# Kernel optimization log

Measured on AMD Instinct MI355X. Metric: run time of the kernel, lower is better.

## Reference

```python
import jax, jax.numpy as jnp
import numpy as np

B, E, H, SEQ = 4096, 512, 512, 128


def setup_inputs() -> dict:
    key = jax.random.key(0)
    ks = jax.random.split(key, 7)
    s = 1.0 / np.sqrt(H)  # PyTorch LSTM init scale
    return {
        "start_emb": jax.random.normal(ks[0], (B, 1, E), dtype=jnp.float32),
        "h0": jax.random.normal(ks[1], (1, B, H), dtype=jnp.float32),
        "c0": jax.random.normal(ks[2], (1, B, H), dtype=jnp.float32),
        "w_ih": jax.random.normal(ks[3], (4 * H, E), dtype=jnp.float32) * s,
        "w_hh": jax.random.normal(ks[4], (4 * H, H), dtype=jnp.float32) * s,
        "b_ih": jax.random.normal(ks[5], (4 * H,), dtype=jnp.float32) * s,
        "b_hh": jax.random.normal(ks[6], (4 * H,), dtype=jnp.float32) * s,
        "seq_length": SEQ,
    }


def reference(start_emb, h0, c0, w_ih, w_hh, b_ih, b_hh, seq_length):
    # start_emb: [B, 1, E] -- identical input every step, so precompute its projection once.
    x = start_emb[:, 0, :]                       # [B, E]
    x_proj = x @ w_ih.T + b_ih + b_hh            # [B, 4H], constant across steps
    hdim = w_hh.shape[1]

    def step(carry, _):
        h, c = carry                              # each [B, H]
        gates = x_proj + h @ w_hh.T               # [B, 4H]
        i, f, g, o = jnp.split(gates, 4, axis=-1) # PyTorch gate order i,f,g,o
        i = jax.nn.sigmoid(i)
        f = jax.nn.sigmoid(f)
        g = jnp.tanh(g)
        o = jax.nn.sigmoid(o)
        c = f * c + i * g
        h = o * jnp.tanh(c)
        return (h, c), None

    (h, c), _ = jax.lax.scan(step, (h0[0], c0[0]), None, length=seq_length)
    # Return final (h_n, c_n) with the [num_layers=1, B, H] leading dim, as PyTorch does.
    return h[None], c[None]
```

## Files before the change

### kernel.cpp

```cpp
#include <hip/hip_runtime.h>
#include <hip/hip_bf16.h>

#define BATCH 4096
#define KD    512
#define NG    2048
#define SEQLEN 128

typedef __attribute__((ext_vector_type(8))) short short8;
typedef __attribute__((ext_vector_type(4))) float floatx4;

#define HWREG_XCC_ID (20 | (0 << 6) | ((4 - 1) << 11))

__device__ __forceinline__ void gld16(const void* g, void* l) {
  __builtin_amdgcn_global_load_lds(
      (const __attribute__((address_space(1))) void*)g,
      (__attribute__((address_space(3))) void*)l, 16, 0, 0);
}

__device__ __forceinline__ float fast_sig(float x) {
  return __builtin_amdgcn_rcpf(1.0f + __expf(-x));
}
__device__ __forceinline__ float fast_tanh(float x) {
  return 1.0f - 2.0f * __builtin_amdgcn_rcpf(1.0f + __expf(2.0f * x));
}

__device__ __forceinline__ unsigned pack_bf16(float lo, float hi) {
  unsigned ul = (unsigned)__builtin_bit_cast(unsigned short, __float2bfloat16(lo));
  unsigned uh = (unsigned)__builtin_bit_cast(unsigned short, __float2bfloat16(hi));
  return (uh << 16) | ul;
}
__device__ __forceinline__ float unpack_lo(unsigned u) {
  u <<= 16; return __builtin_bit_cast(float, u);
}
__device__ __forceinline__ float unpack_hi(unsigned u) {
  u &= 0xffff0000u; return __builtin_bit_cast(float, u);
}

__device__ __forceinline__ void load_panel(const short* __restrict__ W, int bn,
                                           short* __restrict__ lWB, int tid) {
#pragma unroll
  for (int i = 0; i < 16; ++i) {
    int q = i * 512 + tid;
    int row = q >> 6, c = q & 63;
    int c0 = (c & 56) | ((c & 7) ^ (row & 7));
    gld16(W + (size_t)(bn + row) * KD + c0 * 8, lWB + q * 8);
  }
}

__device__ __forceinline__ void gemm_panel(const short* __restrict__ A,
                                           const short* __restrict__ lWB,
                                           short* __restrict__ lA,
                                           floatx4 acc[4][4],
                                           int bm, int lane, int wm, int wn,
                                           int tid) {
#pragma unroll 1
  for (int kt = 0; kt < 8; ++kt) {
    const int k0 = kt * 64;
#pragma unroll
    for (int i = 0; i < 4; ++i) {
      int q = i * 512 + tid;
      int row = q >> 3, cs = q & 7;
      int cc = cs ^ (row & 7);
      gld16(A + (size_t)(bm + row) * KD + k0 + cc * 8, lA + q * 8);
    }
    __syncthreads();
#pragma unroll
    for (int ks = 0; ks < 2; ++ks) {
      short8 a[4], b[4];
#pragma unroll
      for (int mi = 0; mi < 4; ++mi) {
        int arow = wm * 64 + mi * 16 + (lane & 15);
        int ch = (ks * 4 + (lane >> 4)) ^ (arow & 7);
        a[mi] = *(const short8*)&lA[arow * 64 + ch * 8];
      }
#pragma unroll
      for (int j = 0; j < 4; ++j) {
        int brow = wn * 64 + j * 16 + (lane & 15);
        int c = kt * 8 + ks * 4 + (lane >> 4);
        int cc = (c & 56) | ((c & 7) ^ (brow & 7));
        b[j] = *(const short8*)&lWB[brow * 512 + cc * 8];
      }
#pragma unroll
      for (int mi = 0; mi < 4; ++mi)
#pragma unroll
        for (int j = 0; j < 4; ++j)
          acc[mi][j] =
              __builtin_amdgcn_mfma_f32_16x16x32_bf16(a[mi], b[j], acc[mi][j], 0, 0, 0);
    }
    __syncthreads();
  }
}

template <int TBM, int TBN, int NT>
__device__ __forceinline__ void gemm_tile(const short* __restrict__ A,
                                          const short* __restrict__ Bw,
                                          floatx4 acc[4][4],
                                          short* lA, short* lB,
                                          int bm, int bn,
                                          int lane, int wm, int wn, int tid) {
#pragma unroll 1
  for (int kt = 0; kt < KD / 64; ++kt) {
    const int k0 = kt * 64;
#pragma unroll
    for (int i = 0; i < TBM * 8 / NT; ++i) {
      int q = i * NT + tid;
      int row = q >> 3, cs = q & 7;
      int cc = cs ^ (row & 7);
      gld16(A + (size_t)(bm + row) * KD + k0 + cc * 8, lA + q * 8);
    }
#pragma unroll
    for (int i = 0; i < TBN * 8 / NT; ++i) {
      int q = i * NT + tid;
      int row = q >> 3, cs = q & 7;
      int cc = cs ^ (row & 7);
      gld16(Bw + (size_t)(bn + row) * KD + k0 + cc * 8, lB + q * 8);
    }
    __syncthreads();
#pragma unroll
    for (int ks = 0; ks < 2; ++ks) {
      short8 a[4], b[4];
#pragma unroll
      for (int mi = 0; mi < 4; ++mi) {
        int arow = wm * 64 + mi * 16 + (lane & 15);
        int ch = (ks * 4 + (lane >> 4)) ^ (arow & 7);
        a[mi] = *(const short8*)&lA[arow * 64 + ch * 8];
      }
#pragma unroll
      for (int j = 0; j < 4; ++j) {
        int brow = wn * 64 + j * 16 + (lane & 15);
        int ch = (ks * 4 + (lane >> 4)) ^ (brow & 7);
        b[j] = *(const short8*)&lB[brow * 64 + ch * 8];
      }
#pragma unroll
      for (int mi = 0; mi < 4; ++mi)
#pragma unroll
        for (int j = 0; j < 4; ++j)
          acc[mi][j] =
              __builtin_amdgcn_mfma_f32_16x16x32_bf16(a[mi], b[j], acc[mi][j], 0, 0, 0);
    }
    __syncthreads();
  }
}

__device__ __forceinline__ void group_barrier_xcd(unsigned* cnt, unsigned target) {
  __syncthreads();
  if (threadIdx.x == 0) {
    __hip_atomic_fetch_add(cnt, 1u, __ATOMIC_RELAXED, __HIP_MEMORY_SCOPE_AGENT);
    unsigned guard = 0;
    while (__hip_atomic_load(cnt, __ATOMIC_RELAXED, __HIP_MEMORY_SCOPE_AGENT) <
               target &&
           ++guard < (1u << 20)) {
      __builtin_amdgcn_s_sleep(1);
    }
    asm volatile("buffer_inv sc0" ::: "memory");
    asm volatile("s_waitcnt vmcnt(0)" ::: "memory");
  }
  __syncthreads();
}

__global__ __launch_bounds__(512, 1) void lstm_persist(
    const short* __restrict__ xbf,
    const short* __restrict__ wih,
    const short* __restrict__ whh,
    const float* __restrict__ biasp,
    const float* __restrict__ c0,
    short* __restrict__ hA, short* __restrict__ hB,
    float* __restrict__ outH, float* __restrict__ outC,
    unsigned* __restrict__ sync_area) {
  extern __shared__ __align__(16) char dsm[];
  short* lWB = (short*)dsm;
  short* lA  = (short*)(dsm + 131072);

  const int tid = threadIdx.x;
  const int lane = tid & 63;
  const int wid = tid >> 6;
  const int wm = wid >> 1;
  const int wn = wid & 1;

  if (tid == 0) {
    int px = __builtin_amdgcn_s_getreg(HWREG_XCC_ID) & 7;
    unsigned r = __hip_atomic_fetch_add(&sync_area[px], 1u, __ATOMIC_RELAXED,
                                        __HIP_MEMORY_SCOPE_AGENT);
    ((int*)lA)[0] = px * 2 + (int)((r >> 4) & 1);
    ((int*)lA)[1] = (int)(r & 15);
  }
  __syncthreads();
  const int gid = ((int*)lA)[0];
  const int by  = ((int*)lA)[1];
  __syncthreads();
  const int bm = gid * 256;
  const int bn = by * 128;
  unsigned* gcnt = sync_area + 256 + gid * 32;

  const int houter = by * 2 + wn;
  const int hcol = houter * 16 + (lane & 15);
  const int rb = houter * 64 + (lane & 15);

  load_panel(wih, bn, lWB, tid);
  __syncthreads();
  floatx4 acc[4][4] = {};
  gemm_panel(xbf, lWB, lA, acc, bm, lane, wm, wn, tid);

  const float b0 = biasp[rb], b1 = biasp[rb + 16], b2 = biasp[rb + 32],
              b3 = biasp[rb + 48];
  unsigned xprP[4][4][2];
  float creg[4][4];
#pragma unroll
  for (int mi = 0; mi < 4; ++mi) {
    const int mrow0 = bm + wm * 64 + mi * 16 + (lane >> 4) * 4;
#pragma unroll
    for (int reg = 0; reg < 4; ++reg) {
      xprP[mi][reg][0] = pack_bf16(acc[mi][0][reg] + b0, acc[mi][1][reg] + b1);
      xprP[mi][reg][1] = pack_bf16(acc[mi][2][reg] + b2, acc[mi][3][reg] + b3);
      creg[mi][reg] = c0[(size_t)(mrow0 + reg) * KD + hcol];
    }
  }

  load_panel(whh, bn, lWB, tid);
  __syncthreads();

#pragma unroll 1
  for (int t = 0; t < SEQLEN; ++t) {
    const short* hin = (t & 1) ? hB : hA;
    short* hout = (t & 1) ? hA : hB;

#pragma unroll
    for (int mi = 0; mi < 4; ++mi)
#pragma unroll
      for (int j = 0; j < 4; ++j)
        acc[mi][j] = floatx4{0.f, 0.f, 0.f, 0.f};

    gemm_panel(hin, lWB, lA, acc, bm, lane, wm, wn, tid);

#pragma unroll
    for (int mi = 0; mi < 4; ++mi) {
      const int mrow0 = bm + wm * 64 + mi * 16 + (lane >> 4) * 4;
#pragma unroll
      for (int reg = 0; reg < 4; ++reg) {
        const int m = mrow0 + reg;
        float gi = acc[mi][0][reg] + unpack_lo(xprP[mi][reg][0]);
        float gf = acc[mi][1][reg] + unpack_hi(xprP[mi][reg][0]);
        float gg = acc[mi][2][reg] + unpack_lo(xprP[mi][reg][1]);
        float go = acc[mi][3][reg] + unpack_hi(xprP[mi][reg][1]);
        float si = fast_sig(gi);
        float sf = fast_sig(gf);
        float tg = fast_tanh(gg);
        float so = fast_sig(go);
        float cn = sf * creg[mi][reg] + si * tg;
        creg[mi][reg] = cn;
        float hn = so * fast_tanh(cn);
        const size_t ci = (size_t)m * KD + hcol;
        ((__hip_bfloat16*)hout)[ci] = __float2bfloat16(hn);
        if (t == SEQLEN - 1) {
          outH[ci] = hn;
          outC[ci] = cn;
        }
      }
    }
    if (t != SEQLEN - 1) group_barrier_xcd(gcnt, 16u * (unsigned)(t + 1));
  }
}

__global__ __launch_bounds__(256, 2) void lstm_step(
    const short* __restrict__ hin, __hip_bfloat16* __restrict__ hout_bf,
    const short* __restrict__ W, const float* __restrict__ xp,
    float* __restrict__ c, float* __restrict__ hout_f32) {
  __shared__ __align__(16) short lA[128 * 64];
  __shared__ __align__(16) short lB[128 * 64];
  const int tid = threadIdx.x;
  const int lane = tid & 63;
  const int wid = tid >> 6;
  const int wm = wid >> 1, wn = wid & 1;
  const int bm = blockIdx.x * 128, bn = blockIdx.y * 128;

  floatx4 acc[4][4] = {};
  gemm_tile<128, 128, 256>(hin, W, acc, lA, lB, bm, bn, lane, wm, wn, tid);

  const int houter = blockIdx.y * 2 + wn;
  const int hcol = houter * 16 + (lane & 15);
  const int rb = houter * 64 + (lane & 15);
#pragma unroll
  for (int mi = 0; mi < 4; ++mi) {
    const int mrow0 = bm + wm * 64 + mi * 16 + (lane >> 4) * 4;
#pragma unroll
    for (int reg = 0; reg < 4; ++reg) {
      const int m = mrow0 + reg;
      const float* xpr = xp + (size_t)m * NG + rb;
      float si = fast_sig(acc[mi][0][reg] + xpr[0]);
      float sf = fast_sig(acc[mi][1][reg] + xpr[16]);
      float tg = fast_tanh(acc[mi][2][reg] + xpr[32]);
      float so = fast_sig(acc[mi][3][reg] + xpr[48]);
      const int ci = m * KD + hcol;
      float cn = sf * c[ci] + si * tg;
      c[ci] = cn;
      float hn = so * fast_tanh(cn);
      hout_bf[ci] = __float2bfloat16(hn);
      if (hout_f32) hout_f32[ci] = hn;
    }
  }
}

__global__ __launch_bounds__(256, 2) void xproj_gemm(
    const short* __restrict__ xbf, const short* __restrict__ Wih,
    const float* __restrict__ biasp, float* __restrict__ xp) {
  __shared__ __align__(16) short lA[128 * 64];
  __shared__ __align__(16) short lB[128 * 64];
  const int tid = threadIdx.x;
  const int lane = tid & 63;
  const int wid = tid >> 6;
  const int wm = wid >> 1, wn = wid & 1;
  const int bm = blockIdx.x * 128, bn = blockIdx.y * 128;

  floatx4 acc[4][4] = {};
  gemm_tile<128, 128, 256>(xbf, Wih, acc, lA, lB, bm, bn, lane, wm, wn, tid);

  const int houter = blockIdx.y * 2 + wn;
  const int rb = houter * 64 + (lane & 15);
  const float b0 = biasp[rb], b1 = biasp[rb + 16], b2 = biasp[rb + 32],
              b3 = biasp[rb + 48];
#pragma unroll
  for (int mi = 0; mi < 4; ++mi) {
    const int mrow0 = bm + wm * 64 + mi * 16 + (lane >> 4) * 4;
#pragma unroll
    for (int reg = 0; reg < 4; ++reg) {
      float* xpr = xp + (size_t)(mrow0 + reg) * NG + rb;
      xpr[0]  = acc[mi][0][reg] + b0;
      xpr[16] = acc[mi][1][reg] + b1;
      xpr[32] = acc[mi][2][reg] + b2;
      xpr[48] = acc[mi][3][reg] + b3;
    }
  }
}

__global__ void permw_k(const float* __restrict__ w,
                        __hip_bfloat16* __restrict__ o) {
  int idx = blockIdx.x * 256 + threadIdx.x;
  int r = idx >> 9, k = idx & 511;
  int hout = r >> 6, g = (r >> 4) & 3, hin = r & 15;
  o[idx] = __float2bfloat16(w[(size_t)((g << 9) + hout * 16 + hin) * 512 + k]);
}

__global__ void bias_k(const float* __restrict__ bi, const float* __restrict__ bh,
                       float* __restrict__ o) {
  int r = blockIdx.x * 256 + threadIdx.x;
  int hout = r >> 6, g = (r >> 4) & 3, hin = r & 15;
  int n = (g << 9) + hout * 16 + hin;
  o[r] = bi[n] + bh[n];
}

__global__ void f2bf_k(const float* __restrict__ in,
                       __hip_bfloat16* __restrict__ out, int n) {
  int i = blockIdx.x * 256 + threadIdx.x;
  if (i < n) out[i] = __float2bfloat16(in[i]);
}

extern "C" void kernel_launch(void* const* d_in, const int* in_sizes, int n_in,
                              void* d_out, int out_size, void* d_ws, size_t ws_size,
                              hipStream_t stream) {
  const float* start_emb = (const float*)d_in[0];
  const float* h0 = (const float*)d_in[1];
  const float* c0 = (const float*)d_in[2];
  const float* w_ih = (const float*)d_in[3];
  const float* w_hh = (const float*)d_in[4];
  const float* b_ih = (const float*)d_in[5];
  const float* b_hh = (const float*)d_in[6];

  char* ws = (char*)d_ws;
  __hip_bfloat16* whh_p = (__hip_bfloat16*)(ws);
  __hip_bfloat16* wih_p = (__hip_bfloat16*)(ws + (2ll << 20));
  __hip_bfloat16* xbf   = (__hip_bfloat16*)(ws + (4ll << 20));
  __hip_bfloat16* hbufA = (__hip_bfloat16*)(ws + (8ll << 20));
  __hip_bfloat16* hbufB = (__hip_bfloat16*)(ws + (12ll << 20));
  float* biasp          = (float*)(ws + (16ll << 20));
  unsigned* sync_area   = (unsigned*)(ws + (16ll << 20) + 65536);
  float* xp             = (float*)(ws + (17ll << 20));

  float* outH = (float*)d_out;
  float* outC = (float*)d_out + (size_t)BATCH * KD;

  permw_k<<<4096, 256, 0, stream>>>(w_hh, whh_p);
  permw_k<<<4096, 256, 0, stream>>>(w_ih, wih_p);
  bias_k<<<8, 256, 0, stream>>>(b_ih, b_hh, biasp);
  f2bf_k<<<8192, 256, 0, stream>>>(start_emb, xbf, BATCH * KD);
  f2bf_k<<<8192, 256, 0, stream>>>(h0, hbufA, BATCH * KD);
  (void)hipMemsetAsync(sync_area, 0, 8192, stream);

  const short* a_xbf = (const short*)xbf;
  const short* a_wih = (const short*)wih_p;
  const short* a_whh = (const short*)whh_p;
  const float* a_bias = biasp;
  const float* a_c0 = c0;
  short* a_hA = (short*)hbufA;
  short* a_hB = (short*)hbufB;
  float* a_outH = outH;
  float* a_outC = outC;
  unsigned* a_sync = sync_area;
  void* args[] = {&a_xbf, &a_wih, &a_whh, &a_bias, &a_c0,
                  &a_hA, &a_hB, &a_outH, &a_outC, &a_sync};
  hipError_t e = hipLaunchCooperativeKernel((const void*)lstm_persist,
                                            dim3(256), dim3(512), args,
                                            163840, stream);
  if (e != hipSuccess) {
    (void)hipMemcpyAsync(outC, c0, (size_t)BATCH * KD * sizeof(float),
                         hipMemcpyDeviceToDevice, stream);
    dim3 grid(BATCH / 128, NG / 128);
    xproj_gemm<<<grid, 256, 0, stream>>>((const short*)xbf, (const short*)wih_p,
                                         biasp, xp);
    for (int t = 0; t < SEQLEN; ++t) {
      const short* hin = (const short*)((t & 1) ? hbufB : hbufA);
      __hip_bfloat16* hout = (t & 1) ? hbufA : hbufB;
      lstm_step<<<grid, 256, 0, stream>>>(hin, hout, (const short*)whh_p, xp,
                                          outC, (t == SEQLEN - 1) ? outH : nullptr);
    }
  }
}
```

Before: 1.605 ms.

## Keep a quarter of the weight panel in registers and double-buffer A tiles

Each wave now holds one 16-row slice of its recurrent weight panel in VGPRs (16 short8 per lane), and only the remaining 96 rows go to LDS. This shrinks the LDS panel so the A tile can be double-buffered: the next k-tile load is issued before computing on the current one, and the per-k-tile syncthreads pair goes away. The intent is to overlap global-to-LDS loads with MFMA and cut LDS traffic and barriers on the sequential critical path. In exchange register pressure rises a lot, and launch bounds change to 2 blocks, which may force spills. Only one barrier remains after the initial load, so the buffer reuse looks like it could race between k-tiles.

```diff
diff --git a/kernel.cpp b/kernel.cpp
--- a/kernel.cpp
+++ b/kernel.cpp
@@ -36,34 +36,61 @@
   u &= 0xffff0000u; return __builtin_bit_cast(float, u);
 }
 
-__device__ __forceinline__ void load_panel(const short* __restrict__ W, int bn,
-                                           short* __restrict__ lWB, int tid) {
-#pragma unroll
-  for (int i = 0; i < 16; ++i) {
+
+__device__ __forceinline__ void load_panel96(const short* __restrict__ W, int bn,
+                                             short* __restrict__ lWB, int tid) {
+#pragma unroll
+  for (int i = 0; i < 12; ++i) {
     int q = i * 512 + tid;
-    int row = q >> 6, c = q & 63;
-    int c0 = (c & 56) | ((c & 7) ^ (row & 7));
-    gld16(W + (size_t)(bn + row) * KD + c0 * 8, lWB + q * 8);
-  }
-}
-
-__device__ __forceinline__ void gemm_panel(const short* __restrict__ A,
-                                           const short* __restrict__ lWB,
-                                           short* __restrict__ lA,
-                                           floatx4 acc[4][4],
-                                           int bm, int lane, int wm, int wn,
-                                           int tid) {
-#pragma unroll 1
+    int kt = q / 768;
+    int rem = q - kt * 768;
+    int lr = rem >> 3, cc = rem & 7;
+    int cs = cc ^ (lr & 7);
+    int grow = bn + (lr < 48 ? lr + 16 : lr + 32);
+    gld16(W + (size_t)grow * KD + (kt * 8 + cs) * 8, lWB + q * 8);
+  }
+}
+
+__device__ __forceinline__ void load_breg(const short* __restrict__ W, int bn,
+                                          int wn, int lane, short8 breg[16]) {
+  const size_t base = (size_t)(bn + wn * 64 + (lane & 15)) * KD;
+#pragma unroll
+  for (int kt = 0; kt < 8; ++kt)
+#pragma unroll
+    for (int ks = 0; ks < 2; ++ks)
+      breg[kt * 2 + ks] =
+          *(const short8*)&W[base + (size_t)(kt * 8 + ks * 4 + (lane >> 4)) * 8];
+}
+
+__device__ __forceinline__ void gemm_wreg(const short* __restrict__ A,
+                                          const short* __restrict__ lWB,
+                                          short* __restrict__ lAb,
+                                          const short8 breg[16],
+                                          floatx4 acc[4][4],
+                                          int bm, int lane, int wm, int wn,
+                                          int tid) {
+#pragma unroll
+  for (int i = 0; i < 4; ++i) {
+    int q = i * 512 + tid;
+    int row = q >> 3, cs = q & 7;
+    int cc = cs ^ (row & 7);
+    gld16(A + (size_t)(bm + row) * KD + cc * 8, lAb + q * 8);
+  }
+  __syncthreads();
+#pragma unroll
   for (int kt = 0; kt < 8; ++kt) {
-    const int k0 = kt * 64;
-#pragma unroll
-    for (int i = 0; i < 4; ++i) {
-      int q = i * 512 + tid;
-      int row = q >> 3, cs = q & 7;
-      int cc = cs ^ (row & 7);
-      gld16(A + (size_t)(bm + row) * KD + k0 + cc * 8, lA + q * 8);
-    }
-    __syncthreads();
+    const short* curA = lAb + (kt & 1) * 16384;
+    if (kt < 7) {
+      short* nxtA = lAb + ((kt + 1) & 1) * 16384;
+      const int k0 = (kt + 1) * 64;
+#pragma unroll
+      for (int i = 0; i < 4; ++i) {
+        int q = i * 512 + tid;
+        int row = q >> 3, cs = q & 7;
+        int cc = cs ^ (row & 7);
+        gld16(A + (size_t)(bm + row) * KD + k0 + cc * 8, nxtA + q * 8);
+      }
+    }
 #pragma unroll
     for (int ks = 0; ks < 2; ++ks) {
       short8 a[4], b[4];
@@ -71,14 +98,14 @@
       for (int mi = 0; mi < 4; ++mi) {
         int arow = wm * 64 + mi * 16 + (lane & 15);
         int ch = (ks * 4 + (lane >> 4)) ^ (arow & 7);
-        a[mi] = *(const short8*)&lA[arow * 64 + ch * 8];
-      }
-#pragma unroll
-      for (int j = 0; j < 4; ++j) {
-        int brow = wn * 64 + j * 16 + (lane & 15);
-        int c = kt * 8 + ks * 4 + (lane >> 4);
-        int cc = (c & 56) | ((c & 7) ^ (brow & 7));
-        b[j] = *(const short8*)&lWB[brow * 512 + cc * 8];
+        a[mi] = *(const short8*)&curA[arow * 64 + ch * 8];
+      }
+      b[0] = breg[kt * 2 + ks];
+#pragma unroll
+      for (int j = 1; j < 4; ++j) {
+        int lr = wn * 48 + (j - 1) * 16 + (lane & 15);
+        int cc = (ks * 4 + (lane >> 4)) ^ (lr & 7);
+        b[j] = *(const short8*)&lWB[kt * 6144 + lr * 64 + cc * 8];
       }
 #pragma unroll
       for (int mi = 0; mi < 4; ++mi)
@@ -158,7 +185,7 @@
   __syncthreads();
 }
 
-__global__ __launch_bounds__(512, 1) void lstm_persist(
+__global__ __launch_bounds__(512, 2) void lstm_persist(
     const short* __restrict__ xbf,
     const short* __restrict__ wih,
     const short* __restrict__ whh,
@@ -169,7 +196,7 @@
     unsigned* __restrict__ sync_area) {
   extern __shared__ __align__(16) char dsm[];
   short* lWB = (short*)dsm;
-  short* lA  = (short*)(dsm + 131072);
+  short* lAb = (short*)(dsm + 98304);
 
   const int tid = threadIdx.x;
   const int lane = tid & 63;
@@ -181,12 +208,12 @@
     int px = __builtin_amdgcn_s_getreg(HWREG_XCC_ID) & 7;
     unsigned r = __hip_atomic_fetch_add(&sync_area[px], 1u, __ATOMIC_RELAXED,
                                         __HIP_MEMORY_SCOPE_AGENT);
-    ((int*)lA)[0] = px * 2 + (int)((r >> 4) & 1);
-    ((int*)lA)[1] = (int)(r & 15);
-  }
-  __syncthreads();
-  const int gid = ((int*)lA)[0];
-  const int by  = ((int*)lA)[1];
+    ((int*)lAb)[0] = px * 2 + (int)((r >> 4) & 1);
+    ((int*)lAb)[1] = (int)(r & 15);
+  }
+  __syncthreads();
+  const int gid = ((int*)lAb)[0];
+  const int by  = ((int*)lAb)[1];
   __syncthreads();
   const int bm = gid * 256;
   const int bn = by * 128;
@@ -196,10 +223,13 @@
   const int hcol = houter * 16 + (lane & 15);
   const int rb = houter * 64 + (lane & 15);
 
-  load_panel(wih, bn, lWB, tid);
+  short8 breg[16];
+
+  load_panel96(wih, bn, lWB, tid);
+  load_breg(wih, bn, wn, lane, breg);
   __syncthreads();
   floatx4 acc[4][4] = {};
-  gemm_panel(xbf, lWB, lA, acc, bm, lane, wm, wn, tid);
+  gemm_wreg(xbf, lWB, lAb, breg, acc, bm, lane, wm, wn, tid);
 
   const float b0 = biasp[rb], b1 = biasp[rb + 16], b2 = biasp[rb + 32],
               b3 = biasp[rb + 48];
@@ -216,7 +246,8 @@
     }
   }
 
-  load_panel(whh, bn, lWB, tid);
+  load_breg(whh, bn, wn, lane, breg);
+  load_panel96(whh, bn, lWB, tid);
   __syncthreads();
 
 #pragma unroll 1
@@ -230,7 +261,7 @@
       for (int j = 0; j < 4; ++j)
         acc[mi][j] = floatx4{0.f, 0.f, 0.f, 0.f};
 
-    gemm_panel(hin, lWB, lA, acc, bm, lane, wm, wn, tid);
+    gemm_wreg(hin, lWB, lAb, breg, acc, bm, lane, wm, wn, tid);
 
 #pragma unroll
     for (int mi = 0; mi < 4; ++mi) {
```

After: 3.067 ms. 91.1% more time.
